# Optimization experiments

Hardware: AMD Instinct MI355X
Metric: run time of the kernel (lower is better)

## Reference

```python
import jax, jax.numpy as jnp
import numpy as np

OUT_H, OUT_W = 7, 7
SCALE = 0.25
S = 2  # sample_num per bin axis


def _bilinear(img, y, x):
    """Bilinearly sample img[..., H, W] at float coords (y, x).
    y, x have identical shape G; returns img.shape[:-2] + G.
    Matches RoIAlign CUDA interpolation (zero outside [-1, H]/[-1, W])."""
    H, W = img.shape[-2], img.shape[-1]
    valid = (y > -1.0) & (y < H) & (x > -1.0) & (x < W)
    y = jnp.clip(y, 0.0, H - 1)
    x = jnp.clip(x, 0.0, W - 1)
    y0 = jnp.floor(y).astype(jnp.int32)
    x0 = jnp.floor(x).astype(jnp.int32)
    y1 = jnp.minimum(y0 + 1, H - 1)
    x1 = jnp.minimum(x0 + 1, W - 1)
    ly = y - y0
    lx = x - x0
    hy, hx = 1.0 - ly, 1.0 - lx
    v = (hy * hx * img[..., y0, x0] + hy * lx * img[..., y0, x1]
         + ly * hx * img[..., y1, x0] + ly * lx * img[..., y1, x1])
    return jnp.where(valid, v, 0.0)


def setup_inputs() -> dict:
    key = jax.random.key(0)
    k1, k2, k3, k4, k5 = jax.random.split(key, 5)
    N, C, H, W = 2, 256, 200, 200
    R, MH, MW = 512, 128, 128
    features = jax.random.normal(k1, (N, C, H, W), jnp.float32)
    bidx = jax.random.randint(k2, (R,), 0, N)
    xy1 = jax.random.randint(k3, (R, 2), 0, 672)          # x1, y1 (image coords)
    wh = jax.random.randint(k4, (R, 2), 8, 128)           # box sizes in [8,128)
    xy2 = jnp.minimum(xy1 + wh - 1, 799)                  # x2, y2 inclusive
    rois = jnp.concatenate([bidx[:, None].astype(jnp.float32),
                            xy1.astype(jnp.float32),
                            xy2.astype(jnp.float32)], axis=1)  # [R,5]
    batch_masks = jax.random.uniform(k5, (R, MH, MW), jnp.float32)
    # zero-pad beyond each roi's (h, w), mimicking the list->dense packing
    hv = jnp.arange(MH)[None, :] < (xy2[:, 1] - xy1[:, 1] + 1)[:, None]
    wv = jnp.arange(MW)[None, :] < (xy2[:, 0] - xy1[:, 0] + 1)[:, None]
    batch_masks = batch_masks * (hv[:, :, None] & wv[:, None, :]).astype(jnp.float32)
    return {"features": features, "rois": rois, "batch_masks": batch_masks}


def reference(features, rois, batch_masks):
    """Mask-weighted RoIAlign: per-roi bilinear feature samples are weighted by
    the roi's shape mask (bilinearly sampled in roi-relative image coords),
    then average-pooled over the sub-sample grid of each output bin."""
    C = features.shape[1]

    def one_roi(roi, mask):
        b = roi[0].astype(jnp.int32)
        x1, y1, x2, y2 = roi[1], roi[2], roi[3], roi[4]
        roi_start_w = x1 * SCALE
        roi_start_h = y1 * SCALE
        roi_w = jnp.maximum((x2 - x1 + 1.0) * SCALE, 1.0)
        roi_h = jnp.maximum((y2 - y1 + 1.0) * SCALE, 1.0)
        bin_w = roi_w / OUT_W
        bin_h = roi_h / OUT_H
        # sub-sample offsets: (bin + (i+0.5)/S) for i in [0,S)  -> [OUT*S]
        offs = (jnp.arange(S, dtype=jnp.float32) + 0.5) / S
        ys = roi_start_h + (jnp.arange(OUT_H, dtype=jnp.float32)[:, None] + offs[None, :]).reshape(-1) * bin_h
        xs = roi_start_w + (jnp.arange(OUT_W, dtype=jnp.float32)[:, None] + offs[None, :]).reshape(-1) * bin_w
        yy, xx = jnp.meshgrid(ys, xs, indexing='ij')       # [OUT_H*S, OUT_W*S]
        feat = features[b]                                  # [C, H, W]
        vals = _bilinear(feat, yy, xx)                      # [C, OUT_H*S, OUT_W*S]
        # mask weight at the same sample point, in roi-relative image coords
        my = jnp.clip(yy / SCALE - y1, 0.0, y2 - y1)
        mx = jnp.clip(xx / SCALE - x1, 0.0, x2 - x1)
        wgt = _bilinear(mask, my, mx)                       # [OUT_H*S, OUT_W*S]
        v = (vals * wgt).reshape(C, OUT_H, S, OUT_W, S)
        return v.mean(axis=(2, 4))                          # [C, OUT_H, OUT_W]

    return jax.vmap(one_roi)(rois, batch_masks)             # [R, C, OUT_H, OUT_W]
```

## Files before the change

kernel.cpp:

```cpp
#include <hip/hip_runtime.h>


constexpr int   OUT_H = 7, OUT_W = 7;
constexpr int   NBIN  = OUT_H * OUT_W;
constexpr float SCALE = 0.25f;
constexpr int   S     = 2;
constexpr int   NSAMP = NBIN * S * S;
constexpr int   CPB   = 128;

typedef unsigned short ushort_t;

__device__ __forceinline__ ushort_t f2bf(float f) {
    unsigned u = __float_as_uint(f);
    u += 0x7fffu + ((u >> 16) & 1u);
    return (ushort_t)(u >> 16);
}
__device__ __forceinline__ float bf2f(ushort_t h) {
    return __uint_as_float(((unsigned)h) << 16);
}

__global__ __launch_bounds__(256)
void nchw_to_nhwc_bf16_kernel(const float* __restrict__ in,
                              ushort_t* __restrict__ out, int C, int P) {
    __shared__ float tile[64][65];
    const int tx = threadIdx.x;
    const int ty = threadIdx.y;
    const int gx = blockIdx.x * 64;
    const int gy = blockIdx.y * 64;
    const int b  = blockIdx.z;

    const float* inb  = in  + (size_t)b * C * P;
    ushort_t*    outb = out + (size_t)b * C * P;

#pragma unroll
    for (int j = 0; j < 4; ++j) {
        const int c_local = ty + 16 * j;
        const float4 v = *(const float4*)&inb[(size_t)(gy + c_local) * P + gx + 4 * tx];
        tile[c_local][4 * tx + 0] = v.x;
        tile[c_local][4 * tx + 1] = v.y;
        tile[c_local][4 * tx + 2] = v.z;
        tile[c_local][4 * tx + 3] = v.w;
    }
    __syncthreads();
#pragma unroll
    for (int j = 0; j < 4; ++j) {
        const int p_local = ty + 16 * j;
        ushort4 h;
        h.x = f2bf(tile[4 * tx + 0][p_local]);
        h.y = f2bf(tile[4 * tx + 1][p_local]);
        h.z = f2bf(tile[4 * tx + 2][p_local]);
        h.w = f2bf(tile[4 * tx + 3][p_local]);
        *(ushort4*)&outb[(size_t)(gx + p_local) * C + gy + 4 * tx] = h;
    }
}

__global__ __launch_bounds__(256)
void mask_roialign_nhwc_bf16_kernel(const ushort_t* __restrict__ nhwc,
                                    const float* __restrict__ rois,
                                    const float* __restrict__ masks,
                                    float*       __restrict__ out,
                                    int C, int H, int W, int MH, int MW) {
    __shared__ int   s_off[NSAMP][4];
    __shared__ float s_w[NSAMP][4];
    __shared__ float s_out[4][32][NBIN];

    const int r   = blockIdx.x;
    const int cg  = blockIdx.y;
    const int tid = threadIdx.x;

    const float* roi = rois + (size_t)r * 5;
    const int   b  = (int)roi[0];
    const float x1 = roi[1], y1 = roi[2], x2 = roi[3], y2 = roi[4];

    if (tid < NSAMP) {
        const int bin = tid >> 2;
        const int sub = tid & 3;
        const int ph  = bin / OUT_W, pw = bin % OUT_W;
        const int iy  = sub >> 1,   ix = sub & 1;

        const float roi_start_w = x1 * SCALE;
        const float roi_start_h = y1 * SCALE;
        const float roi_w = fmaxf((x2 - x1 + 1.0f) * SCALE, 1.0f);
        const float roi_h = fmaxf((y2 - y1 + 1.0f) * SCALE, 1.0f);
        const float bin_w = roi_w / (float)OUT_W;
        const float bin_h = roi_h / (float)OUT_H;

        const float yy = roi_start_h + ((float)ph + ((float)iy + 0.5f) * (1.0f / S)) * bin_h;
        const float xx = roi_start_w + ((float)pw + ((float)ix + 0.5f) * (1.0f / S)) * bin_w;

        const bool valid = (yy > -1.0f) && (yy < (float)H) && (xx > -1.0f) && (xx < (float)W);

        const float* msk = masks + (size_t)r * MH * MW;
        float my = fminf(fmaxf(yy * (1.0f / SCALE) - y1, 0.0f), y2 - y1);
        float mx = fminf(fmaxf(xx * (1.0f / SCALE) - x1, 0.0f), x2 - x1);
        my = fminf(fmaxf(my, 0.0f), (float)(MH - 1));
        mx = fminf(fmaxf(mx, 0.0f), (float)(MW - 1));
        const int my0 = (int)floorf(my), mx0 = (int)floorf(mx);
        const int my1 = min(my0 + 1, MH - 1), mx1 = min(mx0 + 1, MW - 1);
        const float mly = my - (float)my0, mlx = mx - (float)mx0;
        const float mhy = 1.0f - mly,      mhx = 1.0f - mlx;
        const float wgt = mhy * mhx * msk[my0 * MW + mx0] + mhy * mlx * msk[my0 * MW + mx1]
                        + mly * mhx * msk[my1 * MW + mx0] + mly * mlx * msk[my1 * MW + mx1];

        const float yc = fminf(fmaxf(yy, 0.0f), (float)(H - 1));
        const float xc = fminf(fmaxf(xx, 0.0f), (float)(W - 1));
        const int y0  = (int)floorf(yc), x0 = (int)floorf(xc);
        const int y1i = min(y0 + 1, H - 1), x1i = min(x0 + 1, W - 1);
        const float ly = yc - (float)y0, lx = xc - (float)x0;
        const float hy = 1.0f - ly,      hx = 1.0f - lx;

        const float scale_all = (valid ? wgt : 0.0f) * (1.0f / (float)(S * S));
        s_w[tid][0] = hy * hx * scale_all;
        s_w[tid][1] = hy * lx * scale_all;
        s_w[tid][2] = ly * hx * scale_all;
        s_w[tid][3] = ly * lx * scale_all;
        s_off[tid][0] = (y0  * W + x0 ) * C;
        s_off[tid][1] = (y0  * W + x1i) * C;
        s_off[tid][2] = (y1i * W + x0 ) * C;
        s_off[tid][3] = (y1i * W + x1i) * C;
    }
    __syncthreads();

    const int cq = tid & 31;
    const int bg = tid >> 5;
    const int c0 = cg * CPB + cq * 4;
    const ushort_t* fbase = nhwc + (size_t)b * H * W * C + c0;

    for (int bin = bg; bin < NBIN; bin += 8) {
        float ax = 0.0f, ay = 0.0f, az = 0.0f, aw = 0.0f;
#pragma unroll
        for (int sub = 0; sub < 4; ++sub) {
            const int s = bin * 4 + sub;
            const int   o0 = s_off[s][0], o1 = s_off[s][1], o2 = s_off[s][2], o3 = s_off[s][3];
            const float w0 = s_w[s][0],   w1 = s_w[s][1],   w2 = s_w[s][2],   w3 = s_w[s][3];
            const ushort4 q0 = *(const ushort4*)&fbase[o0];
            const ushort4 q1 = *(const ushort4*)&fbase[o1];
            const ushort4 q2 = *(const ushort4*)&fbase[o2];
            const ushort4 q3 = *(const ushort4*)&fbase[o3];
            ax += w0 * bf2f(q0.x) + w1 * bf2f(q1.x) + w2 * bf2f(q2.x) + w3 * bf2f(q3.x);
            ay += w0 * bf2f(q0.y) + w1 * bf2f(q1.y) + w2 * bf2f(q2.y) + w3 * bf2f(q3.y);
            az += w0 * bf2f(q0.z) + w1 * bf2f(q1.z) + w2 * bf2f(q2.z) + w3 * bf2f(q3.z);
            aw += w0 * bf2f(q0.w) + w1 * bf2f(q1.w) + w2 * bf2f(q2.w) + w3 * bf2f(q3.w);
        }
        s_out[0][cq][bin] = ax;
        s_out[1][cq][bin] = ay;
        s_out[2][cq][bin] = az;
        s_out[3][cq][bin] = aw;
    }
    __syncthreads();

    float* outr = out + ((size_t)r * C + (size_t)cg * CPB) * NBIN;
    for (int i = tid; i < CPB * NBIN; i += 256) {
        const int c   = i / NBIN;
        const int bin = i - c * NBIN;
        outr[i] = s_out[c & 3][c >> 2][bin];
    }
}

__global__ __launch_bounds__(256)
void mask_roialign_kernel(const float* __restrict__ features,
                          const float* __restrict__ rois,
                          const float* __restrict__ masks,
                          float*       __restrict__ out,
                          int C, int H, int W, int MH, int MW) {
    int blk = blockIdx.x;
    int pw  = blk % OUT_W;
    int ph  = (blk / OUT_W) % OUT_H;
    int r   = blk / (OUT_W * OUT_H);
    int c   = threadIdx.x;

    const float* roi = rois + (size_t)r * 5;
    int   b  = (int)roi[0];
    float x1 = roi[1], y1 = roi[2], x2 = roi[3], y2 = roi[4];

    float roi_start_w = x1 * SCALE;
    float roi_start_h = y1 * SCALE;
    float roi_w = fmaxf((x2 - x1 + 1.0f) * SCALE, 1.0f);
    float roi_h = fmaxf((y2 - y1 + 1.0f) * SCALE, 1.0f);
    float bin_w = roi_w / (float)OUT_W;
    float bin_h = roi_h / (float)OUT_H;

    const float* fch = features + ((size_t)b * C + c) * (size_t)(H * W);
    const float* msk = masks + (size_t)r * MH * MW;

    float acc = 0.0f;
#pragma unroll
    for (int iy = 0; iy < S; ++iy) {
        float yy = roi_start_h + ((float)ph + ((float)iy + 0.5f) / (float)S) * bin_h;
#pragma unroll
        for (int ix = 0; ix < S; ++ix) {
            float xx = roi_start_w + ((float)pw + ((float)ix + 0.5f) / (float)S) * bin_w;
            bool valid = (yy > -1.0f) && (yy < (float)H) && (xx > -1.0f) && (xx < (float)W);
            float my = fminf(fmaxf(yy / SCALE - y1, 0.0f), fminf(y2 - y1, (float)(MH - 1)));
            float mx = fminf(fmaxf(xx / SCALE - x1, 0.0f), fminf(x2 - x1, (float)(MW - 1)));
            int my0 = (int)floorf(my), mx0 = (int)floorf(mx);
            int my1 = min(my0 + 1, MH - 1), mx1 = min(mx0 + 1, MW - 1);
            float mly = my - my0, mlx = mx - mx0, mhy = 1.0f - mly, mhx = 1.0f - mlx;
            float wgt = mhy * mhx * msk[my0 * MW + mx0] + mhy * mlx * msk[my0 * MW + mx1]
                      + mly * mhx * msk[my1 * MW + mx0] + mly * mlx * msk[my1 * MW + mx1];
            if (valid) {
                float yc = fminf(fmaxf(yy, 0.0f), (float)(H - 1));
                float xc = fminf(fmaxf(xx, 0.0f), (float)(W - 1));
                int y0 = (int)floorf(yc), x0 = (int)floorf(xc);
                int y1i = min(y0 + 1, H - 1), x1i = min(x0 + 1, W - 1);
                float ly = yc - y0, lx = xc - x0, hy = 1.0f - ly, hx = 1.0f - lx;
                float v = hy * hx * fch[y0  * W + x0 ] + hy * lx * fch[y0  * W + x1i]
                        + ly * hx * fch[y1i * W + x0 ] + ly * lx * fch[y1i * W + x1i];
                acc += wgt * v;
            }
        }
    }
    out[((size_t)r * C + c) * (size_t)NBIN + ph * OUT_W + pw] = acc * (1.0f / (S * S));
}

extern "C" void kernel_launch(void* const* d_in, const int* in_sizes, int n_in,
                              void* d_out, int out_size, void* d_ws, size_t ws_size,
                              hipStream_t stream) {
    const float* features = (const float*)d_in[0];
    const float* rois     = (const float*)d_in[1];
    const float* masks    = (const float*)d_in[2];
    float*       out      = (float*)d_out;

    const int R  = in_sizes[1] / 5;
    const int C  = out_size / (R * NBIN);
    const int H  = 200, W = 200;
    const int MH = 128, MW = 128;
    const int N  = in_sizes[0] / (C * H * W);
    const int P  = H * W;

    const size_t need = (size_t)N * C * P * sizeof(ushort_t);
    const bool tiles_ok = (C % 64 == 0) && (P % 64 == 0) && (C % CPB == 0);
    if (ws_size >= need && tiles_ok) {
        ushort_t* nhwc = (ushort_t*)d_ws;
        dim3 tb(16, 16);
        dim3 tg(P / 64, C / 64, N);
        nchw_to_nhwc_bf16_kernel<<<tg, tb, 0, stream>>>(features, nhwc, C, P);

        mask_roialign_nhwc_bf16_kernel<<<dim3(R, C / CPB), dim3(256), 0, stream>>>(
            nhwc, rois, masks, out, C, H, W, MH, MW);
    } else {
        mask_roialign_kernel<<<dim3(R * NBIN), dim3(256), 0, stream>>>(
            features, rois, masks, out, C, H, W, MH, MW);
    }
}
```

Baseline: 168.3 us.

## Drop NHWC transpose; stage ROI feature window into shared memory per channel group

```diff
diff --git a/kernel.cpp b/kernel.cpp
--- a/kernel.cpp
+++ b/kernel.cpp
@@ -6,7 +6,9 @@
 constexpr float SCALE = 0.25f;
 constexpr int   S     = 2;
 constexpr int   NSAMP = NBIN * S * S;
-constexpr int   CPB   = 128;
+constexpr int   CG    = 32;
+constexpr int   RDIM  = 34;
+constexpr int   RSTRIDE = RDIM * RDIM + 1;
 
 typedef unsigned short ushort_t;
 
@@ -20,49 +22,14 @@
 }
 
 __global__ __launch_bounds__(256)
-void nchw_to_nhwc_bf16_kernel(const float* __restrict__ in,
-                              ushort_t* __restrict__ out, int C, int P) {
-    __shared__ float tile[64][65];
-    const int tx = threadIdx.x;
-    const int ty = threadIdx.y;
-    const int gx = blockIdx.x * 64;
-    const int gy = blockIdx.y * 64;
-    const int b  = blockIdx.z;
-
-    const float* inb  = in  + (size_t)b * C * P;
-    ushort_t*    outb = out + (size_t)b * C * P;
-
-#pragma unroll
-    for (int j = 0; j < 4; ++j) {
-        const int c_local = ty + 16 * j;
-        const float4 v = *(const float4*)&inb[(size_t)(gy + c_local) * P + gx + 4 * tx];
-        tile[c_local][4 * tx + 0] = v.x;
-        tile[c_local][4 * tx + 1] = v.y;
-        tile[c_local][4 * tx + 2] = v.z;
-        tile[c_local][4 * tx + 3] = v.w;
-    }
-    __syncthreads();
-#pragma unroll
-    for (int j = 0; j < 4; ++j) {
-        const int p_local = ty + 16 * j;
-        ushort4 h;
-        h.x = f2bf(tile[4 * tx + 0][p_local]);
-        h.y = f2bf(tile[4 * tx + 1][p_local]);
-        h.z = f2bf(tile[4 * tx + 2][p_local]);
-        h.w = f2bf(tile[4 * tx + 3][p_local]);
-        *(ushort4*)&outb[(size_t)(gx + p_local) * C + gy + 4 * tx] = h;
-    }
-}
-
-__global__ __launch_bounds__(256)
-void mask_roialign_nhwc_bf16_kernel(const ushort_t* __restrict__ nhwc,
-                                    const float* __restrict__ rois,
-                                    const float* __restrict__ masks,
-                                    float*       __restrict__ out,
-                                    int C, int H, int W, int MH, int MW) {
-    __shared__ int   s_off[NSAMP][4];
-    __shared__ float s_w[NSAMP][4];
-    __shared__ float s_out[4][32][NBIN];
+void roialign_direct_kernel(const float* __restrict__ features,
+                            const float* __restrict__ rois,
+                            const float* __restrict__ masks,
+                            float*       __restrict__ out,
+                            int C, int H, int W, int MH, int MW) {
+    __shared__ __align__(16) ushort_t s_reg[CG * RSTRIDE];
+    __shared__ ushort4 s_idx[NSAMP];
+    __shared__ float4  s_w[NSAMP];
 
     const int r   = blockIdx.x;
     const int cg  = blockIdx.y;
@@ -71,19 +38,41 @@
     const float* roi = rois + (size_t)r * 5;
     const int   b  = (int)roi[0];
     const float x1 = roi[1], y1 = roi[2], x2 = roi[3], y2 = roi[4];
+
+    const float roi_start_w = x1 * SCALE;
+    const float roi_start_h = y1 * SCALE;
+    const float roi_w = fmaxf((x2 - x1 + 1.0f) * SCALE, 1.0f);
+    const float roi_h = fmaxf((y2 - y1 + 1.0f) * SCALE, 1.0f);
+    const float bin_w = roi_w * (1.0f / OUT_W);
+    const float bin_h = roi_h * (1.0f / OUT_H);
+
+    int y_lo = (int)floorf(roi_start_h); y_lo = max(0, min(y_lo, H - 1));
+    int x_lo = (int)floorf(roi_start_w); x_lo = max(0, min(x_lo, W - 1));
+    const int y_hi = max(y_lo, min((int)floorf(roi_start_h + roi_h) + 1, H - 1));
+    const int x_hi = max(x_lo, min((int)floorf(roi_start_w + roi_w) + 1, W - 1));
+    const int rows = min(y_hi - y_lo + 1, RDIM);
+    const int cols = min(x_hi - x_lo + 1, RDIM);
+
+    {
+        const int c8  = tid >> 5;
+        const int l32 = tid & 31;
+        const float* fb = features + (size_t)b * C * (size_t)(H * W);
+        for (int cc = c8; cc < CG; cc += 8) {
+            const float* src = fb + (size_t)(cg * CG + cc) * (size_t)(H * W);
+            ushort_t* dst = s_reg + cc * RSTRIDE;
+            for (int ry = 0; ry < rows; ++ry) {
+                const float* rowp = src + (y_lo + ry) * W + x_lo;
+                for (int xk = l32; xk < cols; xk += 32)
+                    dst[ry * RDIM + xk] = f2bf(rowp[xk]);
+            }
+        }
+    }
 
     if (tid < NSAMP) {
         const int bin = tid >> 2;
         const int sub = tid & 3;
         const int ph  = bin / OUT_W, pw = bin % OUT_W;
         const int iy  = sub >> 1,   ix = sub & 1;
-
-        const float roi_start_w = x1 * SCALE;
-        const float roi_start_h = y1 * SCALE;
-        const float roi_w = fmaxf((x2 - x1 + 1.0f) * SCALE, 1.0f);
-        const float roi_h = fmaxf((y2 - y1 + 1.0f) * SCALE, 1.0f);
-        const float bin_w = roi_w / (float)OUT_W;
-        const float bin_h = roi_h / (float)OUT_H;
 
         const float yy = roi_start_h + ((float)ph + ((float)iy + 0.5f) * (1.0f / S)) * bin_h;
         const float xx = roi_start_w + ((float)pw + ((float)ix + 0.5f) * (1.0f / S)) * bin_w;
@@ -109,52 +98,61 @@
         const float ly = yc - (float)y0, lx = xc - (float)x0;
         const float hy = 1.0f - ly,      hx = 1.0f - lx;
 
+        const int ly0 = min(max(y0  - y_lo, 0), RDIM - 1);
+        const int ly1 = min(max(y1i - y_lo, 0), RDIM - 1);
+        const int lx0 = min(max(x0  - x_lo, 0), RDIM - 1);
+        const int lx1 = min(max(x1i - x_lo, 0), RDIM - 1);
+
         const float scale_all = (valid ? wgt : 0.0f) * (1.0f / (float)(S * S));
-        s_w[tid][0] = hy * hx * scale_all;
-        s_w[tid][1] = hy * lx * scale_all;
-        s_w[tid][2] = ly * hx * scale_all;
-        s_w[tid][3] = ly * lx * scale_all;
-        s_off[tid][0] = (y0  * W + x0 ) * C;
-        s_off[tid][1] = (y0  * W + x1i) * C;
-        s_off[tid][2] = (y1i * W + x0 ) * C;
-        s_off[tid][3] = (y1i * W + x1i) * C;
+        ushort4 ix4;
+        ix4.x = (ushort_t)(ly0 * RDIM + lx0);
+        ix4.y = (ushort_t)(ly0 * RDIM + lx1);
+        ix4.z = (ushort_t)(ly1 * RDIM + lx0);
+        ix4.w = (ushort_t)(ly1 * RDIM + lx1);
+        s_idx[tid] = ix4;
+        float4 w4;
+        w4.x = hy * hx * scale_all;
+        w4.y = hy * lx * scale_all;
+        w4.z = ly * hx * scale_all;
+        w4.w = ly * lx * scale_all;
+        s_w[tid] = w4;
     }
     __syncthreads();
 
-    const int cq = tid & 31;
-    const int bg = tid >> 5;
-    const int c0 = cg * CPB + cq * 4;
-    const ushort_t* fbase = nhwc + (size_t)b * H * W * C + c0;
-
-    for (int bin = bg; bin < NBIN; bin += 8) {
-        float ax = 0.0f, ay = 0.0f, az = 0.0f, aw = 0.0f;
-#pragma unroll
-        for (int sub = 0; sub < 4; ++sub) {
-            const int s = bin * 4 + sub;
-            const int   o0 = s_off[s][0], o1 = s_off[s][1], o2 = s_off[s][2], o3 = s_off[s][3];
-            const float w0 = s_w[s][0],   w1 = s_w[s][1],   w2 = s_w[s][2],   w3 = s_w[s][3];
-            const ushort4 q0 = *(const ushort4*)&fbase[o0];
-            const ushort4 q1 = *(const ushort4*)&fbase[o1];
-            const ushort4 q2 = *(const ushort4*)&fbase[o2];
-            const ushort4 q3 = *(const ushort4*)&fbase[o3];
-            ax += w0 * bf2f(q0.x) + w1 * bf2f(q1.x) + w2 * bf2f(q2.x) + w3 * bf2f(q3.x);
-            ay += w0 * bf2f(q0.y) + w1 * bf2f(q1.y) + w2 * bf2f(q2.y) + w3 * bf2f(q3.y);
-            az += w0 * bf2f(q0.z) + w1 * bf2f(q1.z) + w2 * bf2f(q2.z) + w3 * bf2f(q3.z);
-            aw += w0 * bf2f(q0.w) + w1 * bf2f(q1.w) + w2 * bf2f(q2.w) + w3 * bf2f(q3.w);
+    const int c  = tid & 31;
+    const int sg = tid >> 5;
+    const ushort_t* creg = s_reg + c * RSTRIDE;
+
+    float res[7];
+#pragma unroll
+    for (int k = 0; k < 7; ++k) {
+        const int bin = sg + 8 * k;
+        float acc = 0.0f;
+        if (bin < NBIN) {
+#pragma unroll
+            for (int sub = 0; sub < 4; ++sub) {
+                const int s = bin * 4 + sub;
+                const ushort4 ix = s_idx[s];
+                const float4  w  = s_w[s];
+                acc += w.x * bf2f(creg[ix.x]) + w.y * bf2f(creg[ix.y])
+                     + w.z * bf2f(creg[ix.z]) + w.w * bf2f(creg[ix.w]);
+            }
         }
-        s_out[0][cq][bin] = ax;
-        s_out[1][cq][bin] = ay;
-        s_out[2][cq][bin] = az;
-        s_out[3][cq][bin] = aw;
+        res[k] = acc;
     }
     __syncthreads();
 
-    float* outr = out + ((size_t)r * C + (size_t)cg * CPB) * NBIN;
-    for (int i = tid; i < CPB * NBIN; i += 256) {
-        const int c   = i / NBIN;
-        const int bin = i - c * NBIN;
-        outr[i] = s_out[c & 3][c >> 2][bin];
-    }
+    float* s_out = (float*)s_reg;
+#pragma unroll
+    for (int k = 0; k < 7; ++k) {
+        const int bin = sg + 8 * k;
+        if (bin < NBIN) s_out[c * NBIN + bin] = res[k];
+    }
+    __syncthreads();
+
+    float* outr = out + ((size_t)r * C + (size_t)cg * CG) * NBIN;
+    for (int i = tid; i < CG * NBIN; i += 256)
+        outr[i] = s_out[i];
 }
 
 __global__ __launch_bounds__(256)
@@ -168,6 +166,7 @@
     int ph  = (blk / OUT_W) % OUT_H;
     int r   = blk / (OUT_W * OUT_H);
     int c   = threadIdx.x;
+    if (c >= C) return;
 
     const float* roi = rois + (size_t)r * 5;
     int   b  = (int)roi[0];
@@ -225,19 +224,12 @@
     const int C  = out_size / (R * NBIN);
     const int H  = 200, W = 200;
     const int MH = 128, MW = 128;
-    const int N  = in_sizes[0] / (C * H * W);
-    const int P  = H * W;
-
-    const size_t need = (size_t)N * C * P * sizeof(ushort_t);
-    const bool tiles_ok = (C % 64 == 0) && (P % 64 == 0) && (C % CPB == 0);
-    if (ws_size >= need && tiles_ok) {
-        ushort_t* nhwc = (ushort_t*)d_ws;
-        dim3 tb(16, 16);
-        dim3 tg(P / 64, C / 64, N);
-        nchw_to_nhwc_bf16_kernel<<<tg, tb, 0, stream>>>(features, nhwc, C, P);
-
-        mask_roialign_nhwc_bf16_kernel<<<dim3(R, C / CPB), dim3(256), 0, stream>>>(
-            nhwc, rois, masks, out, C, H, W, MH, MW);
+
+    (void)d_ws; (void)ws_size;
+
+    if (C % CG == 0) {
+        roialign_direct_kernel<<<dim3(R, C / CG), dim3(256), 0, stream>>>(
+            features, rois, masks, out, C, H, W, MH, MW);
     } else {
         mask_roialign_kernel<<<dim3(R * NBIN), dim3(256), 0, stream>>>(
             features, rois, masks, out, C, H, W, MH, MW);
```

Measured after the change: 433.8 us. +157.8%, slower.
